# Kernel optimization log

Measured on AMD Instinct MI355X. Metric: run time of the kernel, lower is better.

## Reference

```python
import jax, jax.numpy as jnp
import numpy as np

B, S, D, H = 2, 2048, 1024, 16
DK = D // H


def setup_inputs() -> dict:
    key = jax.random.key(0)
    ks = jax.random.split(key, 8)
    xavier = lambda k, shape: jax.random.uniform(k, shape, jnp.float32, -1.0, 1.0) * np.sqrt(6.0 / (shape[0] + shape[1]))
    return {
        "query": jax.random.normal(ks[0], (B, S, D), jnp.float32),
        "key": jax.random.normal(ks[1], (B, S, D), jnp.float32),
        "value": jax.random.normal(ks[2], (B, S, D), jnp.float32),
        # causal mask: True above the diagonal -> masked out
        "mask": jnp.broadcast_to(jnp.triu(jnp.ones((S, S), bool), k=1), (B, S, S)),
        "w_q": xavier(ks[3], (D, D)),  # torch Linear weight [out, in]
        "w_k": xavier(ks[4], (D, D)),
        "w_v": xavier(ks[5], (D, D)),
        "w_o": xavier(ks[6], (D, D)),
        "b_o": jnp.zeros((D,), jnp.float32),
    }


def reference(query, key, value, mask, w_q, w_k, w_v, w_o, b_o):
    b, sq, d = query.shape
    sk = key.shape[1]
    # projections (torch Linear: x @ W.T)
    Q = (query @ w_q.T).reshape(b, sq, H, DK).transpose(0, 2, 1, 3)  # [B,H,Sq,DK]
    K = (key @ w_k.T).reshape(b, sk, H, DK).transpose(0, 2, 1, 3)
    V = (value @ w_v.T).reshape(b, sk, H, DK).transpose(0, 2, 1, 3)
    scores = jnp.einsum('bhqd,bhkd->bhqk', Q, K) / np.sqrt(DK)
    scores = jnp.where(mask[:, None, :, :], jnp.float32(-1e9), scores)
    attn = jax.nn.softmax(scores, axis=-1)  # dropout is identity in eval
    out = jnp.einsum('bhqk,bhkd->bhqd', attn, V)
    out = out.transpose(0, 2, 1, 3).reshape(b, sq, d)
    return out @ w_o.T + b_o
```

## Files before the change

### kernel.cpp

```cpp
#include <hip/hip_runtime.h>
#include <hip/hip_bf16.h>
#include <stdint.h>


typedef __attribute__((ext_vector_type(4))) float  f32x4;
typedef __attribute__((ext_vector_type(4))) int    i32x4;
typedef __attribute__((ext_vector_type(8))) __bf16 bf16x8;
typedef __attribute__((ext_vector_type(4))) __bf16 bf16x4;
typedef __attribute__((ext_vector_type(2))) __bf16 bf16x2;

#define MFMA16(a, b, c) __builtin_amdgcn_mfma_f32_16x16x32_bf16((a), (b), (c), 0, 0, 0)

__device__ __forceinline__ void async16(const void* g, void* lds) {
  __builtin_amdgcn_global_load_lds(
      (const __attribute__((address_space(1))) uint32_t*)g,
      (__attribute__((address_space(3))) uint32_t*)lds,
      16, 0, 0);
}

__device__ __forceinline__ bf16x8 lds_swz_read(const __bf16* base, int row, int cchunk) {
  const int sw = cchunk ^ (row & 7);
  return *(const bf16x8*)((const char*)base + row * 128 + sw * 16);
}

__global__ void detect_dtype(const uint16_t* __restrict__ w, int* __restrict__ flag) {
  __shared__ int s;
  if (threadIdx.x == 0) s = 0;
  __syncthreads();
  int big = 0;
  for (int i = threadIdx.x; i < 8192; i += 256) {
    uint32_t u = ((uint32_t)w[i]) << 16;
    float f;
    __builtin_memcpy(&f, &u, 4);
    if (fabsf(f) > 1.0f) big = 1;
  }
  if (big) atomicOr(&s, 1);
  __syncthreads();
  if (threadIdx.x == 0) *flag = s;
}

struct CvtArgs { const void* src[8]; void* dst[8]; int n[8]; };

__global__ __launch_bounds__(256)
void convert_all(CvtArgs a, const int* __restrict__ flagp) {
  const int t = blockIdx.y;
  const int n = a.n[t];
  const int i0 = (blockIdx.x * 256 + threadIdx.x) * 8;
  if (i0 >= n) return;
  const int f = *flagp;
  if (f) {
    const float* s = (const float*)a.src[t];
    __bf16* d = (__bf16*)a.dst[t];
    bf16x8 v;
#pragma unroll
    for (int j = 0; j < 8; ++j) v[j] = (__bf16)s[i0 + j];
    *(bf16x8*)(d + i0) = v;
  } else {
    const i32x4* s = (const i32x4*)((const char*)a.src[t] + (size_t)i0 * 2);
    i32x4* d = (i32x4*)((char*)a.dst[t] + (size_t)i0 * 2);
    *d = *s;
  }
}

struct GemmArgs {
  const __bf16* A[3]; const __bf16* W[3]; void* C[3]; float scale[3];
  const __bf16* bias; const int* flagp; int mode;
};

__global__ __launch_bounds__(256, 2)
void gemm_nt(GemmArgs ga)
{
  constexpr int K = 1024;
  __shared__ __align__(16) __bf16 As[128 * 32];
  __shared__ __align__(16) __bf16 Bs[128 * 32];

  const int z = blockIdx.z;
  const __bf16* __restrict__ A = ga.A[z];
  const __bf16* __restrict__ W = ga.W[z];
  void* __restrict__ C = ga.C[z];
  const float scale = ga.scale[z];
  const int mode = ga.mode;

  const int tid = threadIdx.x;
  const int lane = tid & 63;
  const int wave = tid >> 6;
  const int l15 = lane & 15;
  const int quad = lane >> 4;
  const int bm = blockIdx.y * 128;
  const int bn = blockIdx.x * 128;
  const int wm = (wave >> 1) * 64;
  const int wn = (wave & 1) * 64;

  f32x4 acc[4][4];
#pragma unroll
  for (int mi = 0; mi < 4; ++mi)
#pragma unroll
    for (int ni = 0; ni < 4; ++ni) {
      f32x4 zz = {0.f, 0.f, 0.f, 0.f};
      acc[mi][ni] = zz;
    }

  for (int kt = 0; kt < K / 32; ++kt) {
    const int k0 = kt * 32;
    __syncthreads();
#pragma unroll
    for (int r = 0; r < 2; ++r) {
      const int chunk = r * 256 + wave * 64 + lane;
      const int row = chunk >> 2, c = chunk & 3;
      async16(A + (size_t)(bm + row) * K + k0 + c * 8, As + (r * 256 + wave * 64) * 8);
      async16(W + (size_t)(bn + row) * K + k0 + c * 8, Bs + (r * 256 + wave * 64) * 8);
    }
    __syncthreads();

    bf16x8 af[4];
    bf16x8 bfr[4];
#pragma unroll
    for (int mi = 0; mi < 4; ++mi)
      af[mi] = *(const bf16x8*)(As + (wm + mi * 16 + l15) * 32 + quad * 8);
#pragma unroll
    for (int ni = 0; ni < 4; ++ni)
      bfr[ni] = *(const bf16x8*)(Bs + (wn + ni * 16 + l15) * 32 + quad * 8);
#pragma unroll
    for (int mi = 0; mi < 4; ++mi)
#pragma unroll
      for (int ni = 0; ni < 4; ++ni)
        acc[mi][ni] = MFMA16(af[mi], bfr[ni], acc[mi][ni]);
  }

  const int f = (mode == 1) ? *ga.flagp : 0;
#pragma unroll
  for (int ni = 0; ni < 4; ++ni) {
    const int n = bn + wn + ni * 16 + l15;
    const float bv = (mode == 1) ? (float)ga.bias[n] : 0.0f;
#pragma unroll
    for (int mi = 0; mi < 4; ++mi) {
#pragma unroll
      for (int r = 0; r < 4; ++r) {
        const int m = bm + wm + mi * 16 + quad * 4 + r;
        const float v = acc[mi][ni][r] * scale + bv;
        if (mode == 0) {
          const int b = m >> 11, s = m & 2047, h = n >> 6, dk = n & 63;
          ((__bf16*)C)[((size_t)(b * 16 + h) * 2048 + s) * 64 + dk] = (__bf16)v;
        } else if (f) {
          ((float*)C)[(size_t)m * 1024 + n] = v;
        } else {
          ((__bf16*)C)[(size_t)m * 1024 + n] = (__bf16)v;
        }
      }
    }
  }
}

__global__ __launch_bounds__(256, 4)
void attn(const __bf16* __restrict__ Q,
          const __bf16* __restrict__ Kg,
          const __bf16* __restrict__ Vg,
          __bf16* __restrict__ O)
{
  __shared__ __align__(16) __bf16 Qs[64 * 64];
  __shared__ __align__(16) __bf16 Ks[64 * 64];
  __shared__ __align__(16) __bf16 Vts[64][72];
  __shared__ __align__(16) __bf16 PsT[4][16][72];

  const int tid = threadIdx.x;
  const int lane = tid & 63;
  const int wave = tid >> 6;
  const int l15 = lane & 15;
  const int quad = lane >> 4;

  int zb = blockIdx.x, qt, bh;
  if (zb < 512) { qt = zb & 31; bh = zb >> 5; }
  else { int z2 = zb - 512; qt = 31 - (z2 & 31); bh = 16 + (z2 >> 5); }
  const int q0 = qt * 64;

  const __bf16* Qp = Q + (size_t)bh * 2048 * 64;
  const __bf16* Kp = Kg + (size_t)bh * 2048 * 64;
  const __bf16* Vp = Vg + (size_t)bh * 2048 * 64;

#pragma unroll
  for (int r = 0; r < 2; ++r) {
    const int d = r * 256 + wave * 64 + lane;
    const int row = d >> 3, c = (d & 7) ^ (row & 7);
    async16(Qp + (size_t)(q0 + row) * 64 + c * 8, (char*)Qs + (r * 256 + wave * 64) * 16);
  }

  f32x4 o_[4];
#pragma unroll
  for (int dt = 0; dt < 4; ++dt) {
    f32x4 zz = {0.f, 0.f, 0.f, 0.f};
    o_[dt] = zz;
  }
  float mrow = -1e30f, lrow = 0.0f;
  const int qrow = wave * 16 + l15;

  __syncthreads();
  bf16x8 qf[2];
#pragma unroll
  for (int kc = 0; kc < 2; ++kc) qf[kc] = lds_swz_read(Qs, qrow, kc * 4 + quad);

  for (int kt = 0; kt <= qt; ++kt) {
    const int k0 = kt * 64;
    __syncthreads();
#pragma unroll
    for (int r = 0; r < 2; ++r) {
      const int d = r * 256 + wave * 64 + lane;
      const int row = d >> 3, c = (d & 7) ^ (row & 7);
      async16(Kp + (size_t)(k0 + row) * 64 + c * 8, (char*)Ks + (r * 256 + wave * 64) * 16);
    }
    {
      const int kp = tid & 31, dg = tid >> 5;
      bf16x8 v0 = *(const bf16x8*)(Vp + (size_t)(k0 + 2 * kp) * 64 + dg * 8);
      bf16x8 v1 = *(const bf16x8*)(Vp + (size_t)(k0 + 2 * kp + 1) * 64 + dg * 8);
#pragma unroll
      for (int j = 0; j < 8; ++j) {
        bf16x2 pr = { v0[j], v1[j] };
        *(bf16x2*)(&Vts[dg * 8 + j][2 * kp]) = pr;
      }
    }
    __syncthreads();

    f32x4 st[4];
#pragma unroll
    for (int nt = 0; nt < 4; ++nt) {
      f32x4 zz = {0.f, 0.f, 0.f, 0.f};
      st[nt] = zz;
    }
#pragma unroll
    for (int kc = 0; kc < 2; ++kc) {
#pragma unroll
      for (int nt = 0; nt < 4; ++nt) {
        bf16x8 kf = lds_swz_read(Ks, nt * 16 + l15, kc * 4 + quad);
        st[nt] = MFMA16(kf, qf[kc], st[nt]);
      }
    }

    if (kt == qt) {
#pragma unroll
      for (int nt = 0; nt < 4; ++nt)
#pragma unroll
        for (int r = 0; r < 4; ++r)
          if (nt * 16 + quad * 4 + r > qrow) st[nt][r] = -1e30f;
    }

    float tmax = -1e30f;
#pragma unroll
    for (int nt = 0; nt < 4; ++nt)
#pragma unroll
      for (int r = 0; r < 4; ++r) tmax = fmaxf(tmax, st[nt][r]);
    tmax = fmaxf(tmax, __shfl_xor(tmax, 16, 64));
    tmax = fmaxf(tmax, __shfl_xor(tmax, 32, 64));
    const float mnew = fmaxf(mrow, tmax);
    const float alpha = __expf(mrow - mnew);
    float rs = 0.0f;
    bf16x4 pd[4];
#pragma unroll
    for (int nt = 0; nt < 4; ++nt)
#pragma unroll
      for (int r = 0; r < 4; ++r) {
        const float pv = __expf(st[nt][r] - mnew);
        rs += pv;
        pd[nt][r] = (__bf16)pv;
      }
    rs += __shfl_xor(rs, 16, 64);
    rs += __shfl_xor(rs, 32, 64);
    lrow = lrow * alpha + rs;
    mrow = mnew;
#pragma unroll
    for (int dt = 0; dt < 4; ++dt) o_[dt] *= alpha;

#pragma unroll
    for (int nt = 0; nt < 4; ++nt)
      *(bf16x4*)(&PsT[wave][l15][nt * 16 + quad * 4]) = pd[nt];

#pragma unroll
    for (int kc = 0; kc < 2; ++kc) {
      bf16x8 pf = *(const bf16x8*)(&PsT[wave][l15][kc * 32 + quad * 8]);
#pragma unroll
      for (int dt = 0; dt < 4; ++dt) {
        bf16x8 vf = *(const bf16x8*)(&Vts[dt * 16 + l15][kc * 32 + quad * 8]);
        o_[dt] = MFMA16(vf, pf, o_[dt]);
      }
    }
  }

  __syncthreads();
  const float inv_l = 1.0f / lrow;
#pragma unroll
  for (int dt = 0; dt < 4; ++dt)
#pragma unroll
    for (int r = 0; r < 4; r += 2) {
      bf16x2 pr = { (__bf16)(o_[dt][r] * inv_l), (__bf16)(o_[dt][r + 1] * inv_l) };
      *(bf16x2*)(&Vts[wave * 16 + l15][dt * 16 + quad * 4 + r]) = pr;
    }
  __syncthreads();

  const int b = bh >> 4, h = bh & 15;
#pragma unroll
  for (int t = 0; t < 2; ++t) {
    const int i = tid + t * 256;
    const int row = i >> 3, c = i & 7;
    f32x4 v = *(const f32x4*)(&Vts[row][c * 8]);
    *(f32x4*)(O + (size_t)(b * 2048 + q0 + row) * 1024 + h * 64 + c * 8) = v;
  }
}

extern "C" void kernel_launch(void* const* d_in, const int* in_sizes, int n_in,
                              void* d_out, int out_size, void* d_ws, size_t ws_size,
                              hipStream_t stream) {
  char* ws = (char*)d_ws;
  int* flag = (int*)ws;
  __bf16* Xc0 = (__bf16*)(ws + (1u << 20));
  __bf16* Xc1 = (__bf16*)(ws + (9u << 20));
  __bf16* Xc2 = (__bf16*)(ws + (17u << 20));
  __bf16* Wc0 = (__bf16*)(ws + (25u << 20));
  __bf16* Wc1 = (__bf16*)(ws + (27u << 20));
  __bf16* Wc2 = (__bf16*)(ws + (29u << 20));
  __bf16* Wc3 = (__bf16*)(ws + (31u << 20));
  __bf16* bc  = (__bf16*)(ws + (33u << 20));
  __bf16* Qw  = (__bf16*)(ws + (34u << 20));
  __bf16* Kw  = (__bf16*)(ws + (42u << 20));
  __bf16* Vw  = (__bf16*)(ws + (50u << 20));
  __bf16* Aw  = Xc0;

  detect_dtype<<<1, 256, 0, stream>>>((const uint16_t*)d_in[4], flag);

  CvtArgs ca;
  ca.src[0] = d_in[0]; ca.dst[0] = Xc0; ca.n[0] = 4194304;
  ca.src[1] = d_in[1]; ca.dst[1] = Xc1; ca.n[1] = 4194304;
  ca.src[2] = d_in[2]; ca.dst[2] = Xc2; ca.n[2] = 4194304;
  ca.src[3] = d_in[4]; ca.dst[3] = Wc0; ca.n[3] = 1048576;
  ca.src[4] = d_in[5]; ca.dst[4] = Wc1; ca.n[4] = 1048576;
  ca.src[5] = d_in[6]; ca.dst[5] = Wc2; ca.n[5] = 1048576;
  ca.src[6] = d_in[7]; ca.dst[6] = Wc3; ca.n[6] = 1048576;
  ca.src[7] = d_in[8]; ca.dst[7] = bc;  ca.n[7] = 1024;
  convert_all<<<dim3(2048, 8), 256, 0, stream>>>(ca, flag);

  GemmArgs g0;
  g0.A[0] = Xc0; g0.W[0] = Wc0; g0.C[0] = Qw; g0.scale[0] = 0.125f;
  g0.A[1] = Xc1; g0.W[1] = Wc1; g0.C[1] = Kw; g0.scale[1] = 1.0f;
  g0.A[2] = Xc2; g0.W[2] = Wc2; g0.C[2] = Vw; g0.scale[2] = 1.0f;
  g0.bias = nullptr; g0.flagp = flag; g0.mode = 0;
  gemm_nt<<<dim3(8, 32, 3), 256, 0, stream>>>(g0);

  attn<<<dim3(1024), 256, 0, stream>>>(Qw, Kw, Vw, Aw);

  GemmArgs g1;
  g1.A[0] = Aw; g1.W[0] = Wc3; g1.C[0] = d_out; g1.scale[0] = 1.0f;
  g1.A[1] = nullptr; g1.W[1] = nullptr; g1.C[1] = nullptr; g1.scale[1] = 0.f;
  g1.A[2] = nullptr; g1.W[2] = nullptr; g1.C[2] = nullptr; g1.scale[2] = 0.f;
  g1.bias = bc; g1.flagp = flag; g1.mode = 1;
  gemm_nt<<<dim3(8, 32, 1), 256, 0, stream>>>(g1);
}
```

Measured before the change: 252.7 us.

## Process 128 query rows per attention block and double-buffer K/V tiles

Each attention block now covers two 64-row query sub-tiles (128 rows), so every K fragment and V tile loaded from LDS feeds two MFMAs. This halves K/V global and LDS traffic per query. K and V for the next tile are prefetched into a second LDS buffer while the current one is computed, which removes one barrier per iteration. Register pressure goes up, launch bounds drop to 2 blocks per CU, and the grid halves to 512 blocks, so occupancy and load balance across the causal triangle may suffer.

```diff
diff --git a/kernel.cpp b/kernel.cpp
--- a/kernel.cpp
+++ b/kernel.cpp
@@ -151,155 +151,199 @@
   }
 }
 
-__global__ __launch_bounds__(256, 4)
+__global__ __launch_bounds__(256, 2)
 void attn(const __bf16* __restrict__ Q,
           const __bf16* __restrict__ Kg,
           const __bf16* __restrict__ Vg,
           __bf16* __restrict__ O)
 {
-  __shared__ __align__(16) __bf16 Qs[64 * 64];
-  __shared__ __align__(16) __bf16 Ks[64 * 64];
-  __shared__ __align__(16) __bf16 Vts[64][72];
-  __shared__ __align__(16) __bf16 PsT[4][16][72];
+  __shared__ __align__(16) __bf16 PsT[4][2][16][72];
+  __shared__ __align__(16) __bf16 Ks[2][64 * 64];
+  __shared__ __align__(16) __bf16 Vts[2][64][72];
 
   const int tid = threadIdx.x;
   const int lane = tid & 63;
   const int wave = tid >> 6;
   const int l15 = lane & 15;
   const int quad = lane >> 4;
-
-  int zb = blockIdx.x, qt, bh;
-  if (zb < 512) { qt = zb & 31; bh = zb >> 5; }
-  else { int z2 = zb - 512; qt = 31 - (z2 & 31); bh = 16 + (z2 >> 5); }
-  const int q0 = qt * 64;
+  const int kp = tid & 31;
+  const int dg = tid >> 5;
+
+  int zb = blockIdx.x, t, bh;
+  if (zb < 256) { t = zb & 15; bh = zb >> 4; }
+  else { int z2 = zb - 256; t = 15 - (z2 & 15); bh = 16 + (z2 >> 4); }
+  const int q0 = t * 128;
+  const int nIter = 2 * t + 2;
 
   const __bf16* Qp = Q + (size_t)bh * 2048 * 64;
   const __bf16* Kp = Kg + (size_t)bh * 2048 * 64;
   const __bf16* Vp = Vg + (size_t)bh * 2048 * 64;
 
+  __bf16* Qs = &PsT[0][0][0][0];
+
+#pragma unroll
+  for (int r = 0; r < 4; ++r) {
+    const int chunk = r * 256 + tid;
+    const int row = chunk >> 3, c = (chunk & 7) ^ (row & 7);
+    async16(Qp + (size_t)(q0 + row) * 64 + c * 8, (char*)Qs + (r * 256 + wave * 64) * 16);
+  }
 #pragma unroll
   for (int r = 0; r < 2; ++r) {
-    const int d = r * 256 + wave * 64 + lane;
-    const int row = d >> 3, c = (d & 7) ^ (row & 7);
-    async16(Qp + (size_t)(q0 + row) * 64 + c * 8, (char*)Qs + (r * 256 + wave * 64) * 16);
-  }
-
-  f32x4 o_[4];
-#pragma unroll
-  for (int dt = 0; dt < 4; ++dt) {
-    f32x4 zz = {0.f, 0.f, 0.f, 0.f};
-    o_[dt] = zz;
-  }
-  float mrow = -1e30f, lrow = 0.0f;
-  const int qrow = wave * 16 + l15;
-
-  __syncthreads();
-  bf16x8 qf[2];
-#pragma unroll
-  for (int kc = 0; kc < 2; ++kc) qf[kc] = lds_swz_read(Qs, qrow, kc * 4 + quad);
-
-  for (int kt = 0; kt <= qt; ++kt) {
-    const int k0 = kt * 64;
+    const int chunk = r * 256 + tid;
+    const int row = chunk >> 3, c = (chunk & 7) ^ (row & 7);
+    async16(Kp + (size_t)row * 64 + c * 8, (char*)&Ks[0][0] + (r * 256 + wave * 64) * 16);
+  }
+  bf16x8 w0 = *(const bf16x8*)(Vp + (size_t)(2 * kp) * 64 + dg * 8);
+  bf16x8 w1 = *(const bf16x8*)(Vp + (size_t)(2 * kp + 1) * 64 + dg * 8);
+
+  __syncthreads();
+
+#pragma unroll
+  for (int j = 0; j < 8; ++j) {
+    bf16x2 pr = { w0[j], w1[j] };
+    *(bf16x2*)(&Vts[0][dg * 8 + j][2 * kp]) = pr;
+  }
+  const int qrow_wl = wave * 16 + l15;
+  bf16x8 qf[2][2];
+#pragma unroll
+  for (int s = 0; s < 2; ++s)
+#pragma unroll
+    for (int kc = 0; kc < 2; ++kc)
+      qf[s][kc] = lds_swz_read(Qs, s * 64 + qrow_wl, kc * 4 + quad);
+
+  __syncthreads();
+
+  f32x4 o_[2][4];
+#pragma unroll
+  for (int s = 0; s < 2; ++s)
+#pragma unroll
+    for (int dt = 0; dt < 4; ++dt) {
+      f32x4 zz = {0.f, 0.f, 0.f, 0.f};
+      o_[s][dt] = zz;
+    }
+  float mrow[2] = { -1e30f, -1e30f }, lrow[2] = { 0.0f, 0.0f };
+
+  for (int kt = 0; kt < nIter; ++kt) {
+    const int p = kt & 1;
+    const bool pf_on = (kt + 1 < nIter);
+    if (pf_on) {
+      const int kn = (kt + 1) * 64;
+#pragma unroll
+      for (int r = 0; r < 2; ++r) {
+        const int chunk = r * 256 + tid;
+        const int row = chunk >> 3, c = (chunk & 7) ^ (row & 7);
+        async16(Kp + (size_t)(kn + row) * 64 + c * 8,
+                (char*)&Ks[p ^ 1][0] + (r * 256 + wave * 64) * 16);
+      }
+      w0 = *(const bf16x8*)(Vp + (size_t)(kn + 2 * kp) * 64 + dg * 8);
+      w1 = *(const bf16x8*)(Vp + (size_t)(kn + 2 * kp + 1) * 64 + dg * 8);
+    }
+
+    f32x4 st[2][4];
+#pragma unroll
+    for (int s = 0; s < 2; ++s)
+#pragma unroll
+      for (int nt = 0; nt < 4; ++nt) {
+        f32x4 zz = {0.f, 0.f, 0.f, 0.f};
+        st[s][nt] = zz;
+      }
+#pragma unroll
+    for (int kc = 0; kc < 2; ++kc)
+#pragma unroll
+      for (int nt = 0; nt < 4; ++nt) {
+        bf16x8 kf = lds_swz_read(&Ks[p][0], nt * 16 + l15, kc * 4 + quad);
+        st[0][nt] = MFMA16(kf, qf[0][kc], st[0][nt]);
+        st[1][nt] = MFMA16(kf, qf[1][kc], st[1][nt]);
+      }
+
+    if (kt >= 2 * t) {
+#pragma unroll
+      for (int s = 0; s < 2; ++s)
+#pragma unroll
+        for (int nt = 0; nt < 4; ++nt)
+#pragma unroll
+          for (int r = 0; r < 4; ++r)
+            if (64 * kt + nt * 16 + quad * 4 + r > 128 * t + s * 64 + qrow_wl)
+              st[s][nt][r] = -1e30f;
+    }
+
+    float alpha[2];
+#pragma unroll
+    for (int s = 0; s < 2; ++s) {
+      float tmax = -1e30f;
+#pragma unroll
+      for (int nt = 0; nt < 4; ++nt)
+#pragma unroll
+        for (int r = 0; r < 4; ++r) tmax = fmaxf(tmax, st[s][nt][r]);
+      tmax = fmaxf(tmax, __shfl_xor(tmax, 16, 64));
+      tmax = fmaxf(tmax, __shfl_xor(tmax, 32, 64));
+      const float mnew = fmaxf(mrow[s], tmax);
+      alpha[s] = __expf(mrow[s] - mnew);
+      float rs = 0.0f;
+#pragma unroll
+      for (int nt = 0; nt < 4; ++nt) {
+        bf16x4 pd;
+#pragma unroll
+        for (int r = 0; r < 4; ++r) {
+          const float pv = __expf(st[s][nt][r] - mnew);
+          rs += pv;
+          pd[r] = (__bf16)pv;
+        }
+        *(bf16x4*)(&PsT[wave][s][l15][nt * 16 + quad * 4]) = pd;
+      }
+      rs += __shfl_xor(rs, 16, 64);
+      rs += __shfl_xor(rs, 32, 64);
+      lrow[s] = lrow[s] * alpha[s] + rs;
+      mrow[s] = mnew;
+    }
+#pragma unroll
+    for (int s = 0; s < 2; ++s)
+#pragma unroll
+      for (int dt = 0; dt < 4; ++dt) o_[s][dt] *= alpha[s];
+
+#pragma unroll
+    for (int kc = 0; kc < 2; ++kc) {
+      bf16x8 pf0 = *(const bf16x8*)(&PsT[wave][0][l15][kc * 32 + quad * 8]);
+      bf16x8 pf1 = *(const bf16x8*)(&PsT[wave][1][l15][kc * 32 + quad * 8]);
+#pragma unroll
+      for (int dt = 0; dt < 4; ++dt) {
+        bf16x8 vf = *(const bf16x8*)(&Vts[p][dt * 16 + l15][kc * 32 + quad * 8]);
+        o_[0][dt] = MFMA16(vf, pf0, o_[0][dt]);
+        o_[1][dt] = MFMA16(vf, pf1, o_[1][dt]);
+      }
+    }
+
+    if (pf_on) {
+#pragma unroll
+      for (int j = 0; j < 8; ++j) {
+        bf16x2 pr = { w0[j], w1[j] };
+        *(bf16x2*)(&Vts[p ^ 1][dg * 8 + j][2 * kp]) = pr;
+      }
+    }
     __syncthreads();
-#pragma unroll
-    for (int r = 0; r < 2; ++r) {
-      const int d = r * 256 + wave * 64 + lane;
-      const int row = d >> 3, c = (d & 7) ^ (row & 7);
-      async16(Kp + (size_t)(k0 + row) * 64 + c * 8, (char*)Ks + (r * 256 + wave * 64) * 16);
-    }
-    {
-      const int kp = tid & 31, dg = tid >> 5;
-      bf16x8 v0 = *(const bf16x8*)(Vp + (size_t)(k0 + 2 * kp) * 64 + dg * 8);
-      bf16x8 v1 = *(const bf16x8*)(Vp + (size_t)(k0 + 2 * kp + 1) * 64 + dg * 8);
-#pragma unroll
-      for (int j = 0; j < 8; ++j) {
-        bf16x2 pr = { v0[j], v1[j] };
-        *(bf16x2*)(&Vts[dg * 8 + j][2 * kp]) = pr;
-      }
-    }
-    __syncthreads();
-
-    f32x4 st[4];
-#pragma unroll
-    for (int nt = 0; nt < 4; ++nt) {
-      f32x4 zz = {0.f, 0.f, 0.f, 0.f};
-      st[nt] = zz;
-    }
-#pragma unroll
-    for (int kc = 0; kc < 2; ++kc) {
-#pragma unroll
-      for (int nt = 0; nt < 4; ++nt) {
-        bf16x8 kf = lds_swz_read(Ks, nt * 16 + l15, kc * 4 + quad);
-        st[nt] = MFMA16(kf, qf[kc], st[nt]);
-      }
-    }
-
-    if (kt == qt) {
-#pragma unroll
-      for (int nt = 0; nt < 4; ++nt)
-#pragma unroll
-        for (int r = 0; r < 4; ++r)
-          if (nt * 16 + quad * 4 + r > qrow) st[nt][r] = -1e30f;
-    }
-
-    float tmax = -1e30f;
-#pragma unroll
-    for (int nt = 0; nt < 4; ++nt)
-#pragma unroll
-      for (int r = 0; r < 4; ++r) tmax = fmaxf(tmax, st[nt][r]);
-    tmax = fmaxf(tmax, __shfl_xor(tmax, 16, 64));
-    tmax = fmaxf(tmax, __shfl_xor(tmax, 32, 64));
-    const float mnew = fmaxf(mrow, tmax);
-    const float alpha = __expf(mrow - mnew);
-    float rs = 0.0f;
-    bf16x4 pd[4];
-#pragma unroll
-    for (int nt = 0; nt < 4; ++nt)
-#pragma unroll
-      for (int r = 0; r < 4; ++r) {
-        const float pv = __expf(st[nt][r] - mnew);
-        rs += pv;
-        pd[nt][r] = (__bf16)pv;
-      }
-    rs += __shfl_xor(rs, 16, 64);
-    rs += __shfl_xor(rs, 32, 64);
-    lrow = lrow * alpha + rs;
-    mrow = mnew;
-#pragma unroll
-    for (int dt = 0; dt < 4; ++dt) o_[dt] *= alpha;
-
-#pragma unroll
-    for (int nt = 0; nt < 4; ++nt)
-      *(bf16x4*)(&PsT[wave][l15][nt * 16 + quad * 4]) = pd[nt];
-
-#pragma unroll
-    for (int kc = 0; kc < 2; ++kc) {
-      bf16x8 pf = *(const bf16x8*)(&PsT[wave][l15][kc * 32 + quad * 8]);
-#pragma unroll
-      for (int dt = 0; dt < 4; ++dt) {
-        bf16x8 vf = *(const bf16x8*)(&Vts[dt * 16 + l15][kc * 32 + quad * 8]);
-        o_[dt] = MFMA16(vf, pf, o_[dt]);
-      }
-    }
-  }
-
-  __syncthreads();
-  const float inv_l = 1.0f / lrow;
-#pragma unroll
-  for (int dt = 0; dt < 4; ++dt)
-#pragma unroll
-    for (int r = 0; r < 4; r += 2) {
-      bf16x2 pr = { (__bf16)(o_[dt][r] * inv_l), (__bf16)(o_[dt][r + 1] * inv_l) };
-      *(bf16x2*)(&Vts[wave * 16 + l15][dt * 16 + quad * 4 + r]) = pr;
-    }
+  }
+
+  __bf16 (*Ot)[72] = (__bf16(*)[72])&Vts[0][0][0];
+#pragma unroll
+  for (int s = 0; s < 2; ++s) {
+    const float inv_l = 1.0f / lrow[s];
+#pragma unroll
+    for (int dt = 0; dt < 4; ++dt)
+#pragma unroll
+      for (int r = 0; r < 4; r += 2) {
+        bf16x2 pr = { (__bf16)(o_[s][dt][r] * inv_l),
+                      (__bf16)(o_[s][dt][r + 1] * inv_l) };
+        *(bf16x2*)(&Ot[s * 64 + qrow_wl][dt * 16 + quad * 4 + r]) = pr;
+      }
+  }
   __syncthreads();
 
   const int b = bh >> 4, h = bh & 15;
 #pragma unroll
-  for (int t = 0; t < 2; ++t) {
-    const int i = tid + t * 256;
+  for (int r = 0; r < 4; ++r) {
+    const int i = r * 256 + tid;
     const int row = i >> 3, c = i & 7;
-    f32x4 v = *(const f32x4*)(&Vts[row][c * 8]);
+    f32x4 v = *(const f32x4*)(&Ot[row][c * 8]);
     *(f32x4*)(O + (size_t)(b * 2048 + q0 + row) * 1024 + h * 64 + c * 8) = v;
   }
 }
@@ -342,7 +386,7 @@
   g0.bias = nullptr; g0.flagp = flag; g0.mode = 0;
   gemm_nt<<<dim3(8, 32, 3), 256, 0, stream>>>(g0);
 
-  attn<<<dim3(1024), 256, 0, stream>>>(Qw, Kw, Vw, Aw);
+  attn<<<dim3(512), 256, 0, stream>>>(Qw, Kw, Vw, Aw);
 
   GemmArgs g1;
   g1.A[0] = Aw; g1.W[0] = Wc3; g1.C[0] = d_out; g1.scale[0] = 1.0f;
```

Measured after the change: 263.6 us. 4.3% more time.

## Prefetch K into registers and double-buffer V tiles in attention loop

Applied to the files above, without the earlier changes.

Restructures the causal attention kernel so K fragments are loaded straight from global memory into registers, and the next tile's K and V are prefetched while the current tile is computed. V is double-buffered in LDS, so each iteration needs one barrier instead of two, and the Q/K LDS staging buffers are removed. The block ordering also changes to launch the largest query tiles first, to improve load balance. The extra prefetch registers mean the occupancy hint drops from 4 to 3 blocks per SM, which may reduce latency hiding.

```diff
diff --git a/kernel.cpp b/kernel.cpp
--- a/kernel.cpp
+++ b/kernel.cpp
@@ -16,11 +16,6 @@
       (const __attribute__((address_space(1))) uint32_t*)g,
       (__attribute__((address_space(3))) uint32_t*)lds,
       16, 0, 0);
-}
-
-__device__ __forceinline__ bf16x8 lds_swz_read(const __bf16* base, int row, int cchunk) {
-  const int sw = cchunk ^ (row & 7);
-  return *(const bf16x8*)((const char*)base + row * 128 + sw * 16);
 }
 
 __global__ void detect_dtype(const uint16_t* __restrict__ w, int* __restrict__ flag) {
@@ -151,15 +146,13 @@
   }
 }
 
-__global__ __launch_bounds__(256, 4)
+__global__ __launch_bounds__(256, 3)
 void attn(const __bf16* __restrict__ Q,
           const __bf16* __restrict__ Kg,
           const __bf16* __restrict__ Vg,
           __bf16* __restrict__ O)
 {
-  __shared__ __align__(16) __bf16 Qs[64 * 64];
-  __shared__ __align__(16) __bf16 Ks[64 * 64];
-  __shared__ __align__(16) __bf16 Vts[64][72];
+  __shared__ __align__(16) __bf16 Vts[2][64][72];
   __shared__ __align__(16) __bf16 PsT[4][16][72];
 
   const int tid = threadIdx.x;
@@ -167,22 +160,38 @@
   const int wave = tid >> 6;
   const int l15 = lane & 15;
   const int quad = lane >> 4;
-
-  int zb = blockIdx.x, qt, bh;
-  if (zb < 512) { qt = zb & 31; bh = zb >> 5; }
-  else { int z2 = zb - 512; qt = 31 - (z2 & 31); bh = 16 + (z2 >> 5); }
+  const int kp = tid & 31;
+  const int dg = tid >> 5;
+
+  const int zb = blockIdx.x;
+  const int qt = 31 - (zb >> 5);
+  const int bh = zb & 31;
   const int q0 = qt * 64;
 
   const __bf16* Qp = Q + (size_t)bh * 2048 * 64;
   const __bf16* Kp = Kg + (size_t)bh * 2048 * 64;
   const __bf16* Vp = Vg + (size_t)bh * 2048 * 64;
 
-#pragma unroll
-  for (int r = 0; r < 2; ++r) {
-    const int d = r * 256 + wave * 64 + lane;
-    const int row = d >> 3, c = (d & 7) ^ (row & 7);
-    async16(Qp + (size_t)(q0 + row) * 64 + c * 8, (char*)Qs + (r * 256 + wave * 64) * 16);
-  }
+  const int qrow_wl = wave * 16 + l15;
+
+  bf16x8 qf[2], kcur[2][4], knext[2][4];
+#pragma unroll
+  for (int kc = 0; kc < 2; ++kc)
+    qf[kc] = *(const bf16x8*)(Qp + (size_t)(q0 + qrow_wl) * 64 + kc * 32 + quad * 8);
+  bf16x8 w0 = *(const bf16x8*)(Vp + (size_t)(2 * kp) * 64 + dg * 8);
+  bf16x8 w1 = *(const bf16x8*)(Vp + (size_t)(2 * kp + 1) * 64 + dg * 8);
+#pragma unroll
+  for (int kc = 0; kc < 2; ++kc)
+#pragma unroll
+    for (int nt = 0; nt < 4; ++nt)
+      kcur[kc][nt] = *(const bf16x8*)(Kp + (size_t)(nt * 16 + l15) * 64 + kc * 32 + quad * 8);
+
+#pragma unroll
+  for (int j = 0; j < 8; ++j) {
+    bf16x2 pr = { w0[j], w1[j] };
+    *(bf16x2*)(&Vts[0][dg * 8 + j][2 * kp]) = pr;
+  }
+  __syncthreads();
 
   f32x4 o_[4];
 #pragma unroll
@@ -191,33 +200,20 @@
     o_[dt] = zz;
   }
   float mrow = -1e30f, lrow = 0.0f;
-  const int qrow = wave * 16 + l15;
-
-  __syncthreads();
-  bf16x8 qf[2];
-#pragma unroll
-  for (int kc = 0; kc < 2; ++kc) qf[kc] = lds_swz_read(Qs, qrow, kc * 4 + quad);
 
   for (int kt = 0; kt <= qt; ++kt) {
-    const int k0 = kt * 64;
-    __syncthreads();
-#pragma unroll
-    for (int r = 0; r < 2; ++r) {
-      const int d = r * 256 + wave * 64 + lane;
-      const int row = d >> 3, c = (d & 7) ^ (row & 7);
-      async16(Kp + (size_t)(k0 + row) * 64 + c * 8, (char*)Ks + (r * 256 + wave * 64) * 16);
-    }
-    {
-      const int kp = tid & 31, dg = tid >> 5;
-      bf16x8 v0 = *(const bf16x8*)(Vp + (size_t)(k0 + 2 * kp) * 64 + dg * 8);
-      bf16x8 v1 = *(const bf16x8*)(Vp + (size_t)(k0 + 2 * kp + 1) * 64 + dg * 8);
-#pragma unroll
-      for (int j = 0; j < 8; ++j) {
-        bf16x2 pr = { v0[j], v1[j] };
-        *(bf16x2*)(&Vts[dg * 8 + j][2 * kp]) = pr;
-      }
-    }
-    __syncthreads();
+    const int p = kt & 1;
+    const bool pf_on = (kt < qt);
+    if (pf_on) {
+      const int kn = (kt + 1) * 64;
+      w0 = *(const bf16x8*)(Vp + (size_t)(kn + 2 * kp) * 64 + dg * 8);
+      w1 = *(const bf16x8*)(Vp + (size_t)(kn + 2 * kp + 1) * 64 + dg * 8);
+#pragma unroll
+      for (int kc = 0; kc < 2; ++kc)
+#pragma unroll
+        for (int nt = 0; nt < 4; ++nt)
+          knext[kc][nt] = *(const bf16x8*)(Kp + (size_t)(kn + nt * 16 + l15) * 64 + kc * 32 + quad * 8);
+    }
 
     f32x4 st[4];
 #pragma unroll
@@ -226,20 +222,17 @@
       st[nt] = zz;
     }
 #pragma unroll
-    for (int kc = 0; kc < 2; ++kc) {
-#pragma unroll
-      for (int nt = 0; nt < 4; ++nt) {
-        bf16x8 kf = lds_swz_read(Ks, nt * 16 + l15, kc * 4 + quad);
-        st[nt] = MFMA16(kf, qf[kc], st[nt]);
-      }
-    }
+    for (int kc = 0; kc < 2; ++kc)
+#pragma unroll
+      for (int nt = 0; nt < 4; ++nt)
+        st[nt] = MFMA16(kcur[kc][nt], qf[kc], st[nt]);
 
     if (kt == qt) {
 #pragma unroll
       for (int nt = 0; nt < 4; ++nt)
 #pragma unroll
         for (int r = 0; r < 4; ++r)
-          if (nt * 16 + quad * 4 + r > qrow) st[nt][r] = -1e30f;
+          if (nt * 16 + quad * 4 + r > qrow_wl) st[nt][r] = -1e30f;
     }
 
     float tmax = -1e30f;
@@ -252,15 +245,17 @@
     const float mnew = fmaxf(mrow, tmax);
     const float alpha = __expf(mrow - mnew);
     float rs = 0.0f;
-    bf16x4 pd[4];
-#pragma unroll
-    for (int nt = 0; nt < 4; ++nt)
+#pragma unroll
+    for (int nt = 0; nt < 4; ++nt) {
+      bf16x4 pd;
 #pragma unroll
       for (int r = 0; r < 4; ++r) {
         const float pv = __expf(st[nt][r] - mnew);
         rs += pv;
-        pd[nt][r] = (__bf16)pv;
+        pd[r] = (__bf16)pv;
       }
+      *(bf16x4*)(&PsT[wave][l15][nt * 16 + quad * 4]) = pd;
+    }
     rs += __shfl_xor(rs, 16, 64);
     rs += __shfl_xor(rs, 32, 64);
     lrow = lrow * alpha + rs;
@@ -269,37 +264,48 @@
     for (int dt = 0; dt < 4; ++dt) o_[dt] *= alpha;
 
 #pragma unroll
-    for (int nt = 0; nt < 4; ++nt)
-      *(bf16x4*)(&PsT[wave][l15][nt * 16 + quad * 4]) = pd[nt];
-
-#pragma unroll
     for (int kc = 0; kc < 2; ++kc) {
       bf16x8 pf = *(const bf16x8*)(&PsT[wave][l15][kc * 32 + quad * 8]);
 #pragma unroll
       for (int dt = 0; dt < 4; ++dt) {
-        bf16x8 vf = *(const bf16x8*)(&Vts[dt * 16 + l15][kc * 32 + quad * 8]);
+        bf16x8 vf = *(const bf16x8*)(&Vts[p][dt * 16 + l15][kc * 32 + quad * 8]);
         o_[dt] = MFMA16(vf, pf, o_[dt]);
       }
     }
-  }
-
+
+    if (pf_on) {
+#pragma unroll
+      for (int j = 0; j < 8; ++j) {
+        bf16x2 pr = { w0[j], w1[j] };
+        *(bf16x2*)(&Vts[p ^ 1][dg * 8 + j][2 * kp]) = pr;
+      }
+#pragma unroll
+      for (int kc = 0; kc < 2; ++kc)
+#pragma unroll
+        for (int nt = 0; nt < 4; ++nt)
+          kcur[kc][nt] = knext[kc][nt];
+    }
+    __syncthreads();
+  }
+
+  __bf16 (*Ot)[72] = (__bf16(*)[72])&Vts[0][0][0];
+  const float inv_l = 1.0f / lrow;
+#pragma unroll
+  for (int dt = 0; dt < 4; ++dt)
+#pragma unroll
+    for (int r = 0; r < 4; r += 2) {
+      bf16x2 pr = { (__bf16)(o_[dt][r] * inv_l),
+                    (__bf16)(o_[dt][r + 1] * inv_l) };
+      *(bf16x2*)(&Ot[qrow_wl][dt * 16 + quad * 4 + r]) = pr;
+    }
   __syncthreads();
-  const float inv_l = 1.0f / lrow;
-#pragma unroll
-  for (int dt = 0; dt < 4; ++dt)
-#pragma unroll
-    for (int r = 0; r < 4; r += 2) {
-      bf16x2 pr = { (__bf16)(o_[dt][r] * inv_l), (__bf16)(o_[dt][r + 1] * inv_l) };
-      *(bf16x2*)(&Vts[wave * 16 + l15][dt * 16 + quad * 4 + r]) = pr;
-    }
-  __syncthreads();
 
   const int b = bh >> 4, h = bh & 15;
 #pragma unroll
   for (int t = 0; t < 2; ++t) {
-    const int i = tid + t * 256;
+    const int i = t * 256 + tid;
     const int row = i >> 3, c = i & 7;
-    f32x4 v = *(const f32x4*)(&Vts[row][c * 8]);
+    f32x4 v = *(const f32x4*)(&Ot[row][c * 8]);
     *(f32x4*)(O + (size_t)(b * 2048 + q0 + row) * 1024 + h * 64 + c * 8) = v;
   }
 }
```

Result: slower. 292.7 us (+15.8%).
